# Optimization experiments

Measured on AMD Instinct MI355X. Metric: run time of the kernel, lower is better.

The kernel has to match this reference:

```python
import jax, jax.numpy as jnp
import numpy as np

TEMP = 0.05
EPS = 0.1  # label smoothing epsilon (cfg.MODEL.LOSSES.CE.EPSILON)

B, D, N, P = 256, 2048, 65536, 4096


def setup_inputs() -> dict:
    key = jax.random.key(0)
    k1, k2, k3, k4 = jax.random.split(key, 4)
    inputs = jax.random.normal(k1, (B, D), dtype=jnp.float32)
    targets = jax.random.randint(k2, (B,), 0, N)
    prototype = jax.random.normal(k3, (B, P), dtype=jnp.float32)
    features = jax.random.normal(k4, (N, D), dtype=jnp.float32)
    # memory bank rows are kept L2-normalized by the EMA update rule
    features = features / jnp.linalg.norm(features, axis=1, keepdims=True)
    return {"inputs": inputs, "targets": targets, "prototype": prototype, "features": features}


def reference(inputs, targets, prototype, features):
    # F.normalize(inputs, dim=1)
    x = inputs / jnp.linalg.norm(inputs, axis=1, keepdims=True)
    # CM.forward: inputs.mm(features.t())
    mem_logits = x @ features.T                     # [B, N]
    logits = jnp.concatenate([prototype / TEMP, mem_logits / TEMP], axis=1)  # [B, P+N]
    targets_all = targets + prototype.shape[1]
    # label-smoothed cross entropy
    logp = jax.nn.log_softmax(logits, axis=1)       # [B, P+N]
    num_classes = logits.shape[1]
    nll = -jnp.take_along_axis(logp, targets_all[:, None], axis=1)[:, 0]  # [B]
    smooth = -logp.mean(axis=1)                     # [B]
    loss = jnp.mean((1.0 - EPS) * nll + EPS * smooth)
    return loss
```

## Files before the change

kernel.cpp:

```cpp
#include <hip/hip_runtime.h>
#include <stdint.h>

#define M_ROWS 256
#define K_DIM  2048
#define N_FEAT 65536
#define P_PROTO 4096
#define INV_T  20.0f
#define N_CLS  69632.0f
#define BK 32
#define NT 64
#define NBLK (N_FEAT / NT)

typedef __attribute__((ext_vector_type(8))) __bf16 bf16x8;
typedef __attribute__((ext_vector_type(4))) float  f32x4;

__device__ __forceinline__ unsigned short f2bf_rne(float f) {
    unsigned int u = __float_as_uint(f);
    u += 0x7fffu + ((u >> 16) & 1u);
    return (unsigned short)(u >> 16);
}
__device__ __forceinline__ float bf2f(unsigned short u) {
    return __uint_as_float(((unsigned int)u) << 16);
}

__global__ __launch_bounds__(256) void prep_norm(const float* __restrict__ in,
                                                 unsigned short* __restrict__ xb) {
    const int row = blockIdx.x;
    const int tid = threadIdx.x;
    const float4* r = (const float4*)(in + (size_t)row * K_DIM);
    float4 v0 = r[tid];
    float4 v1 = r[tid + 256];
    float ss = v0.x*v0.x + v0.y*v0.y + v0.z*v0.z + v0.w*v0.w
             + v1.x*v1.x + v1.y*v1.y + v1.z*v1.z + v1.w*v1.w;
    #pragma unroll
    for (int off = 32; off; off >>= 1) ss += __shfl_down(ss, off, 64);
    __shared__ float wsum[4];
    if ((tid & 63) == 0) wsum[tid >> 6] = ss;
    __syncthreads();
    float scale = rsqrtf(wsum[0] + wsum[1] + wsum[2] + wsum[3]);

    ushort4 o0, o1;
    o0.x = f2bf_rne(v0.x * scale); o0.y = f2bf_rne(v0.y * scale);
    o0.z = f2bf_rne(v0.z * scale); o0.w = f2bf_rne(v0.w * scale);
    o1.x = f2bf_rne(v1.x * scale); o1.y = f2bf_rne(v1.y * scale);
    o1.z = f2bf_rne(v1.z * scale); o1.w = f2bf_rne(v1.w * scale);
    ushort4* o = (ushort4*)(xb + (size_t)row * K_DIM);
    o[tid]       = o0;
    o[tid + 256] = o1;
}

__global__ __launch_bounds__(256) void tdot(const unsigned short* __restrict__ xb,
                                            const float* __restrict__ feat,
                                            const int* __restrict__ targets,
                                            float* __restrict__ td) {
    const int row = blockIdx.x;
    const int tid = threadIdx.x;
    const int t = targets[row];
    const ushort4* xr = (const ushort4*)(xb + (size_t)row * K_DIM);
    const float4*  fr = (const float4*)(feat + (size_t)t * K_DIM);
    ushort4 xa = xr[tid * 2], xc = xr[tid * 2 + 1];
    float4  fa = fr[tid * 2], fc = fr[tid * 2 + 1];
    float d = bf2f(xa.x) * bf2f(f2bf_rne(fa.x))
            + bf2f(xa.y) * bf2f(f2bf_rne(fa.y))
            + bf2f(xa.z) * bf2f(f2bf_rne(fa.z))
            + bf2f(xa.w) * bf2f(f2bf_rne(fa.w))
            + bf2f(xc.x) * bf2f(f2bf_rne(fc.x))
            + bf2f(xc.y) * bf2f(f2bf_rne(fc.y))
            + bf2f(xc.z) * bf2f(f2bf_rne(fc.z))
            + bf2f(xc.w) * bf2f(f2bf_rne(fc.w));
    #pragma unroll
    for (int off = 32; off; off >>= 1) d += __shfl_down(d, off, 64);
    __shared__ float ws[4];
    if ((tid & 63) == 0) ws[tid >> 6] = d;
    __syncthreads();
    if (tid == 0) td[row] = ws[0] + ws[1] + ws[2] + ws[3];
}

__global__ __launch_bounds__(256) void gemm_fused(const unsigned short* __restrict__ xb,
                                                  const float* __restrict__ feat,
                                                  float* __restrict__ Pm,
                                                  float* __restrict__ Ps,
                                                  float* __restrict__ Psum) {
    __shared__ unsigned short lA[M_ROWS * BK];
    __shared__ unsigned short lB[NT * BK];

    const int tid = threadIdx.x;
    const int w   = tid >> 6;
    const int l   = tid & 63;
    const int lr  = l & 15;
    const int lq  = l >> 4;
    const int n0  = blockIdx.x * NT;

    const unsigned short* agp = xb + (size_t)(w * 64 + (l >> 2)) * K_DIM + (l & 3) * 8;
    const int bn = tid >> 2;
    const int bc = tid & 3;
    const float* fptr = feat + (size_t)(n0 + bn) * K_DIM + bc * 8;
    unsigned short* lbdst = lB + bn * BK + bc * 8;

    const unsigned short* aptr = lA + (size_t)((w * 4) * 16 + lr) * BK + lq * 8;
    const unsigned short* bptr = lB + (size_t)lr * BK + lq * 8;

    f32x4 acc[4][4];
    #pragma unroll
    for (int i = 0; i < 4; ++i)
        #pragma unroll
        for (int j = 0; j < 4; ++j)
            acc[i][j] = (f32x4){0.f, 0.f, 0.f, 0.f};

    for (int kt = 0; kt < K_DIM / BK; ++kt) {
        __syncthreads();
        #pragma unroll
        for (int t = 0; t < 4; ++t) {
            __builtin_amdgcn_global_load_lds(
                (const __attribute__((address_space(1))) void*)(agp + (size_t)t * 16 * K_DIM),
                (__attribute__((address_space(3))) void*)((char*)lA + w * 4096 + t * 1024),
                16, 0, 0);
        }
        float4 f0 = *(const float4*)(fptr);
        float4 f1 = *(const float4*)(fptr + 4);
        uint4 pk;
        pk.x = (unsigned)f2bf_rne(f0.x) | ((unsigned)f2bf_rne(f0.y) << 16);
        pk.y = (unsigned)f2bf_rne(f0.z) | ((unsigned)f2bf_rne(f0.w) << 16);
        pk.z = (unsigned)f2bf_rne(f1.x) | ((unsigned)f2bf_rne(f1.y) << 16);
        pk.w = (unsigned)f2bf_rne(f1.z) | ((unsigned)f2bf_rne(f1.w) << 16);
        *(uint4*)lbdst = pk;
        agp  += BK;
        fptr += BK;
        __syncthreads();

        bf16x8 a[4], b[4];
        #pragma unroll
        for (int i = 0; i < 4; ++i) a[i] = *(const bf16x8*)(aptr + (size_t)i * 16 * BK);
        #pragma unroll
        for (int j = 0; j < 4; ++j) b[j] = *(const bf16x8*)(bptr + (size_t)j * 16 * BK);
        #pragma unroll
        for (int i = 0; i < 4; ++i)
            #pragma unroll
            for (int j = 0; j < 4; ++j)
                acc[i][j] = __builtin_amdgcn_mfma_f32_16x16x32_bf16(a[i], b[j], acc[i][j], 0, 0, 0);
    }

    #pragma unroll
    for (int i = 0; i < 4; ++i) {
        #pragma unroll
        for (int r = 0; r < 4; ++r) {
            float v0 = acc[i][0][r] * INV_T;
            float v1 = acc[i][1][r] * INV_T;
            float v2 = acc[i][2][r] * INV_T;
            float v3 = acc[i][3][r] * INV_T;
            float mx = fmaxf(fmaxf(v0, v1), fmaxf(v2, v3));
            #pragma unroll
            for (int msk = 1; msk < 16; msk <<= 1)
                mx = fmaxf(mx, __shfl_xor(mx, msk, 16));
            float s  = __expf(v0 - mx) + __expf(v1 - mx) + __expf(v2 - mx) + __expf(v3 - mx);
            float sm = v0 + v1 + v2 + v3;
            #pragma unroll
            for (int msk = 1; msk < 16; msk <<= 1) {
                s  += __shfl_xor(s,  msk, 16);
                sm += __shfl_xor(sm, msk, 16);
            }
            if (lr == 0) {
                const int row = (w * 4 + i) * 16 + lq * 4 + r;
                const size_t idx = (size_t)row * NBLK + blockIdx.x;
                Pm[idx] = mx; Ps[idx] = s; Psum[idx] = sm;
            }
        }
    }
}

__global__ __launch_bounds__(256) void row_final(const float* __restrict__ proto,
                                                 const float* __restrict__ Pm,
                                                 const float* __restrict__ Ps,
                                                 const float* __restrict__ Psum,
                                                 const float* __restrict__ td,
                                                 float* __restrict__ rowvals) {
    const int row = blockIdx.x;
    const int tid = threadIdx.x;
    float m = -1.0e30f, s = 0.0f, sum = 0.0f;

    const float* pm = Pm   + (size_t)row * NBLK;
    const float* ps = Ps   + (size_t)row * NBLK;
    const float* pu = Psum + (size_t)row * NBLK;
    #pragma unroll
    for (int k = 0; k < NBLK / 256; ++k) {
        const int b = tid + k * 256;
        float mb = pm[b], sb = ps[b];
        float nm = fmaxf(m, mb);
        s = s * __expf(m - nm) + sb * __expf(mb - nm);
        m = nm;
        sum += pu[b];
    }
    const float4* p4 = (const float4*)(proto + (size_t)row * P_PROTO);
    #pragma unroll
    for (int k = 0; k < P_PROTO / 4 / 256; ++k) {
        float4 v = p4[tid + k * 256];
        float a0 = v.x * INV_T, a1 = v.y * INV_T, a2 = v.z * INV_T, a3 = v.w * INV_T;
        float lm = fmaxf(fmaxf(a0, a1), fmaxf(a2, a3));
        float nm = fmaxf(m, lm);
        s = s * __expf(m - nm)
          + __expf(a0 - nm) + __expf(a1 - nm) + __expf(a2 - nm) + __expf(a3 - nm);
        m = nm;
        sum += a0 + a1 + a2 + a3;
    }

    __shared__ float rm[256], rs[256], rsum[256];
    rm[tid] = m; rs[tid] = s; rsum[tid] = sum;
    __syncthreads();
    #pragma unroll
    for (int off = 128; off; off >>= 1) {
        if (tid < off) {
            float m2 = rm[tid + off], s2 = rs[tid + off];
            float nm = fmaxf(rm[tid], m2);
            rs[tid] = rs[tid] * __expf(rm[tid] - nm) + s2 * __expf(m2 - nm);
            rm[tid] = nm;
            rsum[tid] += rsum[tid + off];
        }
        __syncthreads();
    }
    if (tid == 0) {
        const float lse = rm[0] + __logf(rs[0]);
        const float lt  = td[row] * INV_T;
        rowvals[row] = lse - 0.9f * lt - 0.1f * (rsum[0] / N_CLS);
    }
}

__global__ __launch_bounds__(256) void final_mean(const float* __restrict__ rowvals,
                                                  float* __restrict__ out) {
    const int tid = threadIdx.x;
    float v = rowvals[tid];
    #pragma unroll
    for (int off = 32; off; off >>= 1) v += __shfl_down(v, off, 64);
    __shared__ float ws[4];
    if ((tid & 63) == 0) ws[tid >> 6] = v;
    __syncthreads();
    if (tid == 0) out[0] = (ws[0] + ws[1] + ws[2] + ws[3]) * (1.0f / 256.0f);
}

extern "C" void kernel_launch(void* const* d_in, const int* in_sizes, int n_in,
                              void* d_out, int out_size, void* d_ws, size_t ws_size,
                              hipStream_t stream) {
    const float* inputs  = (const float*)d_in[0];
    const int*   targets = (const int*)d_in[1];
    const float* proto   = (const float*)d_in[2];
    const float* feat    = (const float*)d_in[3];

    char* ws = (char*)d_ws;
    unsigned short* xb = (unsigned short*)ws;
    float* Pm      = (float*)(ws + (1u << 20));
    float* Ps      = (float*)(ws + (2u << 20));
    float* Psum    = (float*)(ws + (3u << 20));
    float* td      = (float*)(ws + (4u << 20));
    float* rowvals = (float*)(ws + (4u << 20) + 4096);
    float* out     = (float*)d_out;

    prep_norm <<<M_ROWS, 256, 0, stream>>>(inputs, xb);
    tdot      <<<M_ROWS, 256, 0, stream>>>(xb, feat, targets, td);
    gemm_fused<<<NBLK,   256, 0, stream>>>(xb, feat, Pm, Ps, Psum);
    row_final <<<M_ROWS, 256, 0, stream>>>(proto, Pm, Ps, Psum, td, rowvals);
    final_mean<<<1,      256, 0, stream>>>(rowvals, out);
}
```

Before: 794.3 us.

## Double GEMM K-tile with XOR-swizzled LDS layout and fuse tdot into prep

```diff
diff --git a/kernel.cpp b/kernel.cpp
--- a/kernel.cpp
+++ b/kernel.cpp
@@ -7,7 +7,7 @@
 #define P_PROTO 4096
 #define INV_T  20.0f
 #define N_CLS  69632.0f
-#define BK 32
+#define BK 64
 #define NT 64
 #define NBLK (N_FEAT / NT)
 
@@ -23,8 +23,11 @@
     return __uint_as_float(((unsigned int)u) << 16);
 }
 
-__global__ __launch_bounds__(256) void prep_norm(const float* __restrict__ in,
-                                                 unsigned short* __restrict__ xb) {
+__global__ __launch_bounds__(256) void prep_tdot(const float* __restrict__ in,
+                                                 const float* __restrict__ feat,
+                                                 const int* __restrict__ targets,
+                                                 unsigned short* __restrict__ xb,
+                                                 float* __restrict__ td) {
     const int row = blockIdx.x;
     const int tid = threadIdx.x;
     const float4* r = (const float4*)(in + (size_t)row * K_DIM);
@@ -47,33 +50,25 @@
     ushort4* o = (ushort4*)(xb + (size_t)row * K_DIM);
     o[tid]       = o0;
     o[tid + 256] = o1;
-}
-
-__global__ __launch_bounds__(256) void tdot(const unsigned short* __restrict__ xb,
-                                            const float* __restrict__ feat,
-                                            const int* __restrict__ targets,
-                                            float* __restrict__ td) {
-    const int row = blockIdx.x;
-    const int tid = threadIdx.x;
+
     const int t = targets[row];
-    const ushort4* xr = (const ushort4*)(xb + (size_t)row * K_DIM);
-    const float4*  fr = (const float4*)(feat + (size_t)t * K_DIM);
-    ushort4 xa = xr[tid * 2], xc = xr[tid * 2 + 1];
-    float4  fa = fr[tid * 2], fc = fr[tid * 2 + 1];
-    float d = bf2f(xa.x) * bf2f(f2bf_rne(fa.x))
-            + bf2f(xa.y) * bf2f(f2bf_rne(fa.y))
-            + bf2f(xa.z) * bf2f(f2bf_rne(fa.z))
-            + bf2f(xa.w) * bf2f(f2bf_rne(fa.w))
-            + bf2f(xc.x) * bf2f(f2bf_rne(fc.x))
-            + bf2f(xc.y) * bf2f(f2bf_rne(fc.y))
-            + bf2f(xc.z) * bf2f(f2bf_rne(fc.z))
-            + bf2f(xc.w) * bf2f(f2bf_rne(fc.w));
+    const float4* fr = (const float4*)(feat + (size_t)t * K_DIM);
+    float4 fa = fr[tid];
+    float4 fc = fr[tid + 256];
+    float d = bf2f(o0.x) * bf2f(f2bf_rne(fa.x))
+            + bf2f(o0.y) * bf2f(f2bf_rne(fa.y))
+            + bf2f(o0.z) * bf2f(f2bf_rne(fa.z))
+            + bf2f(o0.w) * bf2f(f2bf_rne(fa.w))
+            + bf2f(o1.x) * bf2f(f2bf_rne(fc.x))
+            + bf2f(o1.y) * bf2f(f2bf_rne(fc.y))
+            + bf2f(o1.z) * bf2f(f2bf_rne(fc.z))
+            + bf2f(o1.w) * bf2f(f2bf_rne(fc.w));
     #pragma unroll
     for (int off = 32; off; off >>= 1) d += __shfl_down(d, off, 64);
-    __shared__ float ws[4];
-    if ((tid & 63) == 0) ws[tid >> 6] = d;
-    __syncthreads();
-    if (tid == 0) td[row] = ws[0] + ws[1] + ws[2] + ws[3];
+    __shared__ float wd[4];
+    if ((tid & 63) == 0) wd[tid >> 6] = d;
+    __syncthreads();
+    if (tid == 0) td[row] = wd[0] + wd[1] + wd[2] + wd[3];
 }
 
 __global__ __launch_bounds__(256) void gemm_fused(const unsigned short* __restrict__ xb,
@@ -89,16 +84,22 @@
     const int l   = tid & 63;
     const int lr  = l & 15;
     const int lq  = l >> 4;
+    const int sw  = lr & 7;
     const int n0  = blockIdx.x * NT;
 
-    const unsigned short* agp = xb + (size_t)(w * 64 + (l >> 2)) * K_DIM + (l & 3) * 8;
+    const unsigned short* agp = xb
+        + (size_t)(w * 8 + (l >> 3)) * K_DIM
+        + (((l & 7) ^ ((l >> 3) & 7)) << 3);
+
     const int bn = tid >> 2;
     const int bc = tid & 3;
-    const float* fptr = feat + (size_t)(n0 + bn) * K_DIM + bc * 8;
-    unsigned short* lbdst = lB + bn * BK + bc * 8;
-
-    const unsigned short* aptr = lA + (size_t)((w * 4) * 16 + lr) * BK + lq * 8;
-    const unsigned short* bptr = lB + (size_t)lr * BK + lq * 8;
+    const float* fptr = feat + (size_t)(n0 + bn) * K_DIM + bc * 16;
+    char* lbrow = (char*)lB + bn * 128;
+    const int p0 = (((bc * 2)     ^ (bn & 7)) << 4);
+    const int p1 = (((bc * 2 + 1) ^ (bn & 7)) << 4);
+
+    const char* lab = (const char*)lA + (size_t)(w * 64 + lr) * 128;
+    const char* lbb = (const char*)lB + (size_t)lr * 128;
 
     f32x4 acc[4][4];
     #pragma unroll
@@ -110,34 +111,45 @@
     for (int kt = 0; kt < K_DIM / BK; ++kt) {
         __syncthreads();
         #pragma unroll
-        for (int t = 0; t < 4; ++t) {
+        for (int t = 0; t < 8; ++t) {
             __builtin_amdgcn_global_load_lds(
-                (const __attribute__((address_space(1))) void*)(agp + (size_t)t * 16 * K_DIM),
-                (__attribute__((address_space(3))) void*)((char*)lA + w * 4096 + t * 1024),
+                (const __attribute__((address_space(1))) void*)(agp + (size_t)t * 32 * K_DIM),
+                (__attribute__((address_space(3))) void*)((char*)lA + (t * 32 + w * 8) * 128),
                 16, 0, 0);
         }
         float4 f0 = *(const float4*)(fptr);
         float4 f1 = *(const float4*)(fptr + 4);
-        uint4 pk;
-        pk.x = (unsigned)f2bf_rne(f0.x) | ((unsigned)f2bf_rne(f0.y) << 16);
-        pk.y = (unsigned)f2bf_rne(f0.z) | ((unsigned)f2bf_rne(f0.w) << 16);
-        pk.z = (unsigned)f2bf_rne(f1.x) | ((unsigned)f2bf_rne(f1.y) << 16);
-        pk.w = (unsigned)f2bf_rne(f1.z) | ((unsigned)f2bf_rne(f1.w) << 16);
-        *(uint4*)lbdst = pk;
+        float4 f2 = *(const float4*)(fptr + 8);
+        float4 f3 = *(const float4*)(fptr + 12);
+        uint4 ua, ub;
+        ua.x = (unsigned)f2bf_rne(f0.x) | ((unsigned)f2bf_rne(f0.y) << 16);
+        ua.y = (unsigned)f2bf_rne(f0.z) | ((unsigned)f2bf_rne(f0.w) << 16);
+        ua.z = (unsigned)f2bf_rne(f1.x) | ((unsigned)f2bf_rne(f1.y) << 16);
+        ua.w = (unsigned)f2bf_rne(f1.z) | ((unsigned)f2bf_rne(f1.w) << 16);
+        ub.x = (unsigned)f2bf_rne(f2.x) | ((unsigned)f2bf_rne(f2.y) << 16);
+        ub.y = (unsigned)f2bf_rne(f2.z) | ((unsigned)f2bf_rne(f2.w) << 16);
+        ub.z = (unsigned)f2bf_rne(f3.x) | ((unsigned)f2bf_rne(f3.y) << 16);
+        ub.w = (unsigned)f2bf_rne(f3.z) | ((unsigned)f2bf_rne(f3.w) << 16);
+        *(uint4*)(lbrow + p0) = ua;
+        *(uint4*)(lbrow + p1) = ub;
         agp  += BK;
         fptr += BK;
         __syncthreads();
 
-        bf16x8 a[4], b[4];
-        #pragma unroll
-        for (int i = 0; i < 4; ++i) a[i] = *(const bf16x8*)(aptr + (size_t)i * 16 * BK);
-        #pragma unroll
-        for (int j = 0; j < 4; ++j) b[j] = *(const bf16x8*)(bptr + (size_t)j * 16 * BK);
-        #pragma unroll
-        for (int i = 0; i < 4; ++i)
-            #pragma unroll
-            for (int j = 0; j < 4; ++j)
-                acc[i][j] = __builtin_amdgcn_mfma_f32_16x16x32_bf16(a[i], b[j], acc[i][j], 0, 0, 0);
+        #pragma unroll
+        for (int kk = 0; kk < 2; ++kk) {
+            const int ct = (((kk * 4 + lq) ^ sw) << 4);
+            bf16x8 a[4], b[4];
+            #pragma unroll
+            for (int i = 0; i < 4; ++i) a[i] = *(const bf16x8*)(lab + i * 2048 + ct);
+            #pragma unroll
+            for (int j = 0; j < 4; ++j) b[j] = *(const bf16x8*)(lbb + j * 2048 + ct);
+            #pragma unroll
+            for (int i = 0; i < 4; ++i)
+                #pragma unroll
+                for (int j = 0; j < 4; ++j)
+                    acc[i][j] = __builtin_amdgcn_mfma_f32_16x16x32_bf16(a[i], b[j], acc[i][j], 0, 0, 0);
+        }
     }
 
     #pragma unroll
@@ -253,8 +265,7 @@
     float* rowvals = (float*)(ws + (4u << 20) + 4096);
     float* out     = (float*)d_out;
 
-    prep_norm <<<M_ROWS, 256, 0, stream>>>(inputs, xb);
-    tdot      <<<M_ROWS, 256, 0, stream>>>(xb, feat, targets, td);
+    prep_tdot <<<M_ROWS, 256, 0, stream>>>(inputs, feat, targets, xb, td);
     gemm_fused<<<NBLK,   256, 0, stream>>>(xb, feat, Pm, Ps, Psum);
     row_final <<<M_ROWS, 256, 0, stream>>>(proto, Pm, Ps, Psum, td, rowvals);
     final_mean<<<1,      256, 0, stream>>>(rowvals, out);
```

Result: faster. 738.1 us (-7.1%).
